# Optimization experiments

Hardware: AMD Instinct MI355X
Metric: run time of the kernel (lower is better)

## Reference

```python
import jax, jax.numpy as jnp
import numpy as np

B, C, R, D = 32, 30, 196, 256
K = 20            # max_det_per_class
CONF = 0.5        # conf_threshold
IOU_THR = 0.3     # iou_threshold


def setup_inputs() -> dict:
    key = jax.random.key(0)
    k1, k2, k3 = jax.random.split(key, 3)
    return {
        "local_features": jax.random.normal(k1, (B, C, R, D), dtype=jnp.float32),
        "W_coords": jax.random.normal(k2, (4, D), dtype=jnp.float32) * 0.02,
        "b_coords": jnp.zeros((4,), jnp.float32),
        "W_pres": jax.random.normal(k3, (1, D), dtype=jnp.float32) * 0.02,
        "b_pres": jnp.zeros((1,), jnp.float32),
    }


def _grid_centers_xyxy(num_regions):
    # centers of a GxG grid in normalized coords, repeated to width 4 (xyxy)
    g = int(round(np.sqrt(num_regions)))
    assert g * g == num_regions
    c = (np.arange(g, dtype=np.float32) + 0.5) / g
    cy, cx = np.meshgrid(c, c, indexing="ij")
    centers = np.stack([cx, cy], axis=-1).reshape(-1, 2)  # [R, 2]
    return jnp.asarray(np.tile(centers, (1, 2)))          # [R, 4]


def _pairwise_iou(boxes):
    # boxes: [K, 4] xyxy -> [K, K]
    x1, y1, x2, y2 = boxes[:, 0], boxes[:, 1], boxes[:, 2], boxes[:, 3]
    area = jnp.clip(x2 - x1, 0) * jnp.clip(y2 - y1, 0)
    xx1 = jnp.maximum(x1[:, None], x1[None, :])
    yy1 = jnp.maximum(y1[:, None], y1[None, :])
    xx2 = jnp.minimum(x2[:, None], x2[None, :])
    yy2 = jnp.minimum(y2[:, None], y2[None, :])
    inter = jnp.clip(xx2 - xx1, 0) * jnp.clip(yy2 - yy1, 0)
    union = area[:, None] + area[None, :] - inter
    return inter / jnp.maximum(union, 1e-9)


def _nms_keep(boxes, valid):
    # boxes: [K, 4] already sorted by descending score; valid: [K] bool
    iou = _pairwise_iou(boxes)
    later = jnp.arange(K)

    def body(i, keep):
        sup = keep[i] & (iou[i] > IOU_THR) & (later > i)
        return keep & (~sup)

    return jax.lax.fori_loop(0, K, body, valid)


def _forward(local_features, W_coords, b_coords, W_pres, b_pres):
    # Linear heads: [B, C, R, D] -> [B, C, R, 4] and [B, C, R, 1]
    coords = jnp.einsum("bcrd,od->bcro", local_features, W_coords) + b_coords
    presence = jnp.einsum("bcrd,od->bcro", local_features, W_pres) + b_pres
    probs = jax.nn.sigmoid(presence[..., 0])  # [B, C, R]

    # predict_relative with xyxy format: add grid centers
    coords = coords + _grid_centers_xyxy(R)[None, None]

    # top-k per (image, class); top_k returns scores sorted descending
    probs_k, idx = jax.lax.top_k(probs, K)                      # [B, C, K]
    coords_k = jnp.take_along_axis(coords, idx[..., None], axis=2)  # [B, C, K, 4]

    # confidence threshold (padded mask instead of dynamic shapes)
    valid = probs_k > CONF

    # per-(image, class) greedy NMS; class shift in original => class-separable
    keep = jax.vmap(jax.vmap(_nms_keep))(coords_k, valid)       # [B, C, K] bool
    kf = keep.astype(coords_k.dtype)
    coords_out = coords_k * kf[..., None]
    probs_out = probs_k * kf
    return coords_out, probs_out, keep, presence


def reference(local_features, W_coords, b_coords, W_pres, b_pres):
    return _forward(local_features, W_coords, b_coords, W_pres, b_pres)
```

## Files before the change

kernel.cpp:

```cpp
#include <hip/hip_runtime.h>
#include <hip/hip_bf16.h>
#include <math.h>

#define BB 32
#define CC 30
#define RR 196
#define DD 256
#define KK 20
#define GG 14
#define CONF_ 0.5f
#define IOU_THR_ 0.3f

constexpr int COORDS_OFF = 0;
constexpr int PROBS_OFF  = BB * CC * KK * 4;
constexpr int KEEP_OFF   = PROBS_OFF + BB * CC * KK;
constexpr int PRES_OFF   = KEEP_OFF + BB * CC * KK;

__device__ __forceinline__ float dot4(float4 a, float4 b) {
    return a.x * b.x + a.y * b.y + a.z * b.z + a.w * b.w;
}

__global__ __launch_bounds__(256, 4) void fused_bbox_lean(
    const float4* __restrict__ lf,
    const float*  __restrict__ W_coords,
    const float*  __restrict__ b_coords,
    const float*  __restrict__ W_pres,
    const float*  __restrict__ b_pres,
    float* __restrict__ coords_out,
    float* __restrict__ probs_out,
    float* __restrict__ keep_out,
    float* __restrict__ presence_out)
{
    const int bc   = blockIdx.x;
    const int tid  = threadIdx.x;
    const int wv   = tid >> 6;
    const int lane = tid & 63;
    const int gr   = lane >> 4;
    const int o    = lane & 15;

    __shared__ float  s_logit[RR];
    __shared__ float4 s_box[RR];

    const float4* __restrict__ Wp4 = reinterpret_cast<const float4*>(W_pres);
    const float4* __restrict__ Wc4 = reinterpret_cast<const float4*>(W_coords);

    float4 wp[4], w0[4], w1[4], w2[4], w3[4];
    #pragma unroll
    for (int t = 0; t < 4; ++t) {
        wp[t] = Wp4[o + 16 * t];
        w0[t] = Wc4[      o + 16 * t];
        w1[t] = Wc4[ 64 + o + 16 * t];
        w2[t] = Wc4[128 + o + 16 * t];
        w3[t] = Wc4[192 + o + 16 * t];
    }
    const float bp  = b_pres[0];
    const float bc0 = b_coords[0], bc1 = b_coords[1];
    const float bc2 = b_coords[2], bc3 = b_coords[3];

    const size_t tile  = (size_t)bc * RR;
    const int    wbase = wv * 49;

    #pragma unroll 1
    for (int j = 0; j < 12; ++j) {
        const int r = wbase + 4 * j + gr;
        const float4* __restrict__ rp = lf + (tile + r) * 64;

        float ap = 0.f, a0 = 0.f, a1 = 0.f, a2 = 0.f, a3 = 0.f;
        #pragma unroll
        for (int t = 0; t < 4; ++t) {
            const float4 x = rp[o + 16 * t];
            ap += dot4(x, wp[t]);
            a0 += dot4(x, w0[t]);
            a1 += dot4(x, w1[t]);
            a2 += dot4(x, w2[t]);
            a3 += dot4(x, w3[t]);
        }
        #pragma unroll
        for (int off = 1; off <= 8; off <<= 1) {
            ap += __shfl_xor(ap, off);
            a0 += __shfl_xor(a0, off);
            a1 += __shfl_xor(a1, off);
            a2 += __shfl_xor(a2, off);
            a3 += __shfl_xor(a3, off);
        }
        if (o == 0) {
            const float lg = ap + bp;
            s_logit[r] = lg;
            presence_out[tile + r] = lg;
            const int   ix = r % GG, iy = r / GG;
            const float cx = (ix + 0.5f) / (float)GG;
            const float cy = (iy + 0.5f) / (float)GG;
            s_box[r] = make_float4(a0 + bc0 + cx, a1 + bc1 + cy,
                                   a2 + bc2 + cx, a3 + bc3 + cy);
        }
    }

    if (gr == 0) {
        const int r = wbase + 48;
        const float4* __restrict__ rp = lf + (tile + r) * 64;
        float ap = 0.f, a0 = 0.f, a1 = 0.f, a2 = 0.f, a3 = 0.f;
        #pragma unroll
        for (int t = 0; t < 4; ++t) {
            const float4 x = rp[o + 16 * t];
            ap += dot4(x, wp[t]);
            a0 += dot4(x, w0[t]);
            a1 += dot4(x, w1[t]);
            a2 += dot4(x, w2[t]);
            a3 += dot4(x, w3[t]);
        }
        #pragma unroll
        for (int off = 1; off <= 8; off <<= 1) {
            ap += __shfl_xor(ap, off);
            a0 += __shfl_xor(a0, off);
            a1 += __shfl_xor(a1, off);
            a2 += __shfl_xor(a2, off);
            a3 += __shfl_xor(a3, off);
        }
        if (o == 0) {
            const float lg = ap + bp;
            s_logit[r] = lg;
            presence_out[tile + r] = lg;
            const int   ix = r % GG, iy = r / GG;
            const float cx = (ix + 0.5f) / (float)GG;
            const float cy = (iy + 0.5f) / (float)GG;
            s_box[r] = make_float4(a0 + bc0 + cx, a1 + bc1 + cy,
                                   a2 + bc2 + cx, a3 + bc3 + cy);
        }
    }

    __syncthreads();
    if (wv != 0) return;

    float v[4]; int id[4];
    #pragma unroll
    for (int t = 0; t < 4; ++t) {
        const int r = lane + 64 * t;
        id[t] = r;
        v[t]  = (r < RR) ? s_logit[r] : -1e30f;
    }

    float myv = -1e30f; int myi = 0;
    for (int k = 0; k < KK; ++k) {
        float bv = v[0]; int bi = id[0];
        #pragma unroll
        for (int t = 1; t < 4; ++t)
            if (v[t] > bv || (v[t] == bv && id[t] < bi)) { bv = v[t]; bi = id[t]; }
        #pragma unroll
        for (int off = 32; off; off >>= 1) {
            const float ov = __shfl_xor(bv, off);
            const int   oi = __shfl_xor(bi, off);
            if (ov > bv || (ov == bv && oi < bi)) { bv = ov; bi = oi; }
        }
        #pragma unroll
        for (int t = 0; t < 4; ++t)
            if (id[t] == bi) v[t] = -1e30f;
        if (lane == k) { myv = bv; myi = bi; }
    }

    float x1 = 0.f, y1 = 0.f, x2 = 0.f, y2 = 0.f, area = 0.f, prob = 0.f;
    int kp = 0;
    if (lane < KK) {
        const float4 b = s_box[myi];
        x1 = b.x; y1 = b.y; x2 = b.z; y2 = b.w;
        area = fmaxf(x2 - x1, 0.f) * fmaxf(y2 - y1, 0.f);
        prob = 1.f / (1.f + expf(-myv));
        kp   = (prob > CONF_) ? 1 : 0;
    }
    for (int i = 0; i < KK; ++i) {
        const int   ki  = __shfl(kp, i);
        const float bx1 = __shfl(x1, i), by1 = __shfl(y1, i);
        const float bx2 = __shfl(x2, i), by2 = __shfl(y2, i);
        const float ai  = __shfl(area, i);
        if (lane > i && lane < KK && ki) {
            const float xx1 = fmaxf(x1, bx1), yy1 = fmaxf(y1, by1);
            const float xx2 = fminf(x2, bx2), yy2 = fminf(y2, by2);
            const float inter = fmaxf(xx2 - xx1, 0.f) * fmaxf(yy2 - yy1, 0.f);
            const float uni   = area + ai - inter;
            const float iou   = inter / fmaxf(uni, 1e-9f);
            if (iou > IOU_THR_) kp = 0;
        }
    }

    if (lane < KK) {
        const size_t base = (size_t)bc * KK + lane;
        const float  kf   = kp ? 1.f : 0.f;
        coords_out[base * 4 + 0] = x1 * kf;
        coords_out[base * 4 + 1] = y1 * kf;
        coords_out[base * 4 + 2] = x2 * kf;
        coords_out[base * 4 + 3] = y2 * kf;
        probs_out[base] = prob * kf;
        keep_out[base]  = kf;
    }
}

extern "C" void kernel_launch(void* const* d_in, const int* in_sizes, int n_in,
                              void* d_out, int out_size, void* d_ws, size_t ws_size,
                              hipStream_t stream) {
    const float* lf       = (const float*)d_in[0];
    const float* W_coords = (const float*)d_in[1];
    const float* b_coords = (const float*)d_in[2];
    const float* W_pres   = (const float*)d_in[3];
    const float* b_pres   = (const float*)d_in[4];

    float* out          = (float*)d_out;
    float* coords_out   = out + COORDS_OFF;
    float* probs_out    = out + PROBS_OFF;
    float* keep_out     = out + KEEP_OFF;
    float* presence_out = out + PRES_OFF;

    fused_bbox_lean<<<BB * CC, 256, 0, stream>>>(
        (const float4*)lf, W_coords, b_coords, W_pres, b_pres,
        coords_out, probs_out, keep_out, presence_out);
}
```

Baseline: 50.46 us.

## Software-pipeline row loads with 4-deep register prefetch and 32-lane rows

After: 59.00 us. +16.9%, slower.

```diff
diff --git a/kernel.cpp b/kernel.cpp
--- a/kernel.cpp
+++ b/kernel.cpp
@@ -20,7 +20,7 @@
     return a.x * b.x + a.y * b.y + a.z * b.z + a.w * b.w;
 }
 
-__global__ __launch_bounds__(256, 4) void fused_bbox_lean(
+__global__ __launch_bounds__(256, 4) void fused_bbox_deep(
     const float4* __restrict__ lf,
     const float*  __restrict__ W_coords,
     const float*  __restrict__ b_coords,
@@ -35,8 +35,8 @@
     const int tid  = threadIdx.x;
     const int wv   = tid >> 6;
     const int lane = tid & 63;
-    const int gr   = lane >> 4;
-    const int o    = lane & 15;
+    const int o2   = lane & 31;
+    const int hr   = lane >> 5;
 
     __shared__ float  s_logit[RR];
     __shared__ float4 s_box[RR];
@@ -44,82 +44,99 @@
     const float4* __restrict__ Wp4 = reinterpret_cast<const float4*>(W_pres);
     const float4* __restrict__ Wc4 = reinterpret_cast<const float4*>(W_coords);
 
-    float4 wp[4], w0[4], w1[4], w2[4], w3[4];
-    #pragma unroll
-    for (int t = 0; t < 4; ++t) {
-        wp[t] = Wp4[o + 16 * t];
-        w0[t] = Wc4[      o + 16 * t];
-        w1[t] = Wc4[ 64 + o + 16 * t];
-        w2[t] = Wc4[128 + o + 16 * t];
-        w3[t] = Wc4[192 + o + 16 * t];
-    }
+    const float4 wp0 = Wp4[o2],        wp1 = Wp4[o2 + 32];
+    const float4 wa0 = Wc4[o2],        wa1 = Wc4[o2 + 32];
+    const float4 wb0 = Wc4[64 + o2],   wb1 = Wc4[96 + o2];
+    const float4 wc0 = Wc4[128 + o2],  wc1 = Wc4[160 + o2];
+    const float4 wd0 = Wc4[192 + o2],  wd1 = Wc4[224 + o2];
+
     const float bp  = b_pres[0];
     const float bc0 = b_coords[0], bc1 = b_coords[1];
     const float bc2 = b_coords[2], bc3 = b_coords[3];
 
-    const size_t tile  = (size_t)bc * RR;
-    const int    wbase = wv * 49;
+    const size_t tileRows = (size_t)bc * RR;
+    const float4* __restrict__ tp = lf + tileRows * 64;
+    const int base = wv * 49;
+
+#define LOADG(X0, X1, g)                                                 \
+    {                                                                    \
+        const float4* __restrict__ _p = tp + (size_t)(base + 2*(g) + hr) * 64; \
+        X0 = _p[o2];                                                     \
+        X1 = _p[o2 + 32];                                                \
+    }
+
+#define COMPG(g, X0, X1)                                                 \
+    {                                                                    \
+        float ap = dot4(X0, wp0) + dot4(X1, wp1);                        \
+        float a0 = dot4(X0, wa0) + dot4(X1, wa1);                        \
+        float a1 = dot4(X0, wb0) + dot4(X1, wb1);                        \
+        float a2 = dot4(X0, wc0) + dot4(X1, wc1);                        \
+        float a3 = dot4(X0, wd0) + dot4(X1, wd1);                        \
+        _Pragma("unroll")                                                \
+        for (int off = 1; off <= 16; off <<= 1) {                        \
+            ap += __shfl_xor(ap, off);                                   \
+            a0 += __shfl_xor(a0, off);                                   \
+            a1 += __shfl_xor(a1, off);                                   \
+            a2 += __shfl_xor(a2, off);                                   \
+            a3 += __shfl_xor(a3, off);                                   \
+        }                                                                \
+        if (o2 == 0) {                                                   \
+            const int r = base + 2*(g) + hr;                             \
+            const float lg = ap + bp;                                    \
+            s_logit[r] = lg;                                             \
+            presence_out[tileRows + r] = lg;                             \
+            const int   ix = r % GG, iy = r / GG;                        \
+            const float cx = (ix + 0.5f) / (float)GG;                    \
+            const float cy = (iy + 0.5f) / (float)GG;                    \
+            s_box[r] = make_float4(a0 + bc0 + cx, a1 + bc1 + cy,         \
+                                   a2 + bc2 + cx, a3 + bc3 + cy);        \
+        }                                                                \
+    }
+
+    float4 t0, t1;
+    {
+        const float4* __restrict__ _p = tp + (size_t)(base + 48) * 64;
+        t0 = _p[o2];
+        t1 = _p[o2 + 32];
+    }
+
+    float4 A0, A1, B0, B1, C0, C1, D0, D1;
+    LOADG(A0, A1, 0)
+    LOADG(B0, B1, 1)
+    LOADG(C0, C1, 2)
+    LOADG(D0, D1, 3)
 
     #pragma unroll 1
-    for (int j = 0; j < 12; ++j) {
-        const int r = wbase + 4 * j + gr;
-        const float4* __restrict__ rp = lf + (tile + r) * 64;
-
-        float ap = 0.f, a0 = 0.f, a1 = 0.f, a2 = 0.f, a3 = 0.f;
-        #pragma unroll
-        for (int t = 0; t < 4; ++t) {
-            const float4 x = rp[o + 16 * t];
-            ap += dot4(x, wp[t]);
-            a0 += dot4(x, w0[t]);
-            a1 += dot4(x, w1[t]);
-            a2 += dot4(x, w2[t]);
-            a3 += dot4(x, w3[t]);
-        }
-        #pragma unroll
-        for (int off = 1; off <= 8; off <<= 1) {
+    for (int it = 0; it < 24; it += 4) {
+        COMPG(it,     A0, A1)
+        if (it + 4 < 24) LOADG(A0, A1, it + 4)
+        COMPG(it + 1, B0, B1)
+        if (it + 5 < 24) LOADG(B0, B1, it + 5)
+        COMPG(it + 2, C0, C1)
+        if (it + 6 < 24) LOADG(C0, C1, it + 6)
+        COMPG(it + 3, D0, D1)
+        if (it + 7 < 24) LOADG(D0, D1, it + 7)
+    }
+
+    {
+        float ap = dot4(t0, wp0) + dot4(t1, wp1);
+        float a0 = dot4(t0, wa0) + dot4(t1, wa1);
+        float a1 = dot4(t0, wb0) + dot4(t1, wb1);
+        float a2 = dot4(t0, wc0) + dot4(t1, wc1);
+        float a3 = dot4(t0, wd0) + dot4(t1, wd1);
+        #pragma unroll
+        for (int off = 1; off <= 16; off <<= 1) {
             ap += __shfl_xor(ap, off);
             a0 += __shfl_xor(a0, off);
             a1 += __shfl_xor(a1, off);
             a2 += __shfl_xor(a2, off);
             a3 += __shfl_xor(a3, off);
         }
-        if (o == 0) {
+        if (lane == 0) {
+            const int r = base + 48;
             const float lg = ap + bp;
             s_logit[r] = lg;
-            presence_out[tile + r] = lg;
-            const int   ix = r % GG, iy = r / GG;
-            const float cx = (ix + 0.5f) / (float)GG;
-            const float cy = (iy + 0.5f) / (float)GG;
-            s_box[r] = make_float4(a0 + bc0 + cx, a1 + bc1 + cy,
-                                   a2 + bc2 + cx, a3 + bc3 + cy);
-        }
-    }
-
-    if (gr == 0) {
-        const int r = wbase + 48;
-        const float4* __restrict__ rp = lf + (tile + r) * 64;
-        float ap = 0.f, a0 = 0.f, a1 = 0.f, a2 = 0.f, a3 = 0.f;
-        #pragma unroll
-        for (int t = 0; t < 4; ++t) {
-            const float4 x = rp[o + 16 * t];
-            ap += dot4(x, wp[t]);
-            a0 += dot4(x, w0[t]);
-            a1 += dot4(x, w1[t]);
-            a2 += dot4(x, w2[t]);
-            a3 += dot4(x, w3[t]);
-        }
-        #pragma unroll
-        for (int off = 1; off <= 8; off <<= 1) {
-            ap += __shfl_xor(ap, off);
-            a0 += __shfl_xor(a0, off);
-            a1 += __shfl_xor(a1, off);
-            a2 += __shfl_xor(a2, off);
-            a3 += __shfl_xor(a3, off);
-        }
-        if (o == 0) {
-            const float lg = ap + bp;
-            s_logit[r] = lg;
-            presence_out[tile + r] = lg;
+            presence_out[tileRows + r] = lg;
             const int   ix = r % GG, iy = r / GG;
             const float cx = (ix + 0.5f) / (float)GG;
             const float cy = (iy + 0.5f) / (float)GG;
@@ -182,15 +199,17 @@
     }
 
     if (lane < KK) {
-        const size_t base = (size_t)bc * KK + lane;
-        const float  kf   = kp ? 1.f : 0.f;
-        coords_out[base * 4 + 0] = x1 * kf;
-        coords_out[base * 4 + 1] = y1 * kf;
-        coords_out[base * 4 + 2] = x2 * kf;
-        coords_out[base * 4 + 3] = y2 * kf;
-        probs_out[base] = prob * kf;
-        keep_out[base]  = kf;
-    }
+        const size_t obase = (size_t)bc * KK + lane;
+        const float  kf    = kp ? 1.f : 0.f;
+        coords_out[obase * 4 + 0] = x1 * kf;
+        coords_out[obase * 4 + 1] = y1 * kf;
+        coords_out[obase * 4 + 2] = x2 * kf;
+        coords_out[obase * 4 + 3] = y2 * kf;
+        probs_out[obase] = prob * kf;
+        keep_out[obase]  = kf;
+    }
+#undef LOADG
+#undef COMPG
 }
 
 extern "C" void kernel_launch(void* const* d_in, const int* in_sizes, int n_in,
@@ -208,7 +227,7 @@
     float* keep_out     = out + KEEP_OFF;
     float* presence_out = out + PRES_OFF;
 
-    fused_bbox_lean<<<BB * CC, 256, 0, stream>>>(
+    fused_bbox_deep<<<BB * CC, 256, 0, stream>>>(
         (const float4*)lf, W_coords, b_coords, W_pres, b_pres,
         coords_out, probs_out, keep_out, presence_out);
 }
```
